# Kernel optimization log

Measured on AMD Instinct MI355X. Metric: run time of the kernel, lower is better.

Reference implementation:

```python
import jax, jax.numpy as jnp
import numpy as np
from jax import lax

NUM_CLS = 58

def _bsign(a):
    # BNN sign: +1 for a >= 0, -1 otherwise
    return jnp.where(a >= 0, 1.0, -1.0).astype(a.dtype)

def _conv(x, w, stride=1):
    return lax.conv_general_dilated(
        x, w, window_strides=(stride, stride), padding='VALID',
        dimension_numbers=('NCHW', 'OIHW', 'NCHW'))

def _binconv(x, w):
    # BinaryConv2d: binarize activations and weights via sign, then conv
    return _conv(_bsign(x), _bsign(w))

def _maxpool(x, k=2, s=2):
    return lax.reduce_window(x, -jnp.inf, lax.max,
                             (1, 1, k, k), (1, 1, s, s), 'VALID')

def setup_inputs() -> dict:
    key = jax.random.key(0)
    ks = jax.random.split(key, 7)
    B = 1024
    x = jax.random.normal(ks[0], (B, 3, 32, 32), dtype=jnp.float32)
    w0 = jax.random.normal(ks[1], (128, 3, 3, 3), dtype=jnp.float32) * 0.1   # float conv
    w1 = jax.random.normal(ks[2], (128, 128, 3, 3), dtype=jnp.float32) * 0.1 # binary conv
    w2 = jax.random.normal(ks[3], (128, 128, 3, 3), dtype=jnp.float32) * 0.1 # binary conv
    w3 = jax.random.normal(ks[4], (128, 128, 3, 3), dtype=jnp.float32) * 0.1 # binary conv
    w4 = jax.random.normal(ks[5], (128, 128, 1, 1), dtype=jnp.float32) * 0.1 # binary 1x1
    w5 = jax.random.normal(ks[6], (NUM_CLS, 128, 1, 1), dtype=jnp.float32) * 0.1  # float 1x1
    return {'x': x, 'w0': w0, 'w1': w1, 'w2': w2, 'w3': w3, 'w4': w4, 'w5': w5}

def reference(x, w0, w1, w2, w3, w4, w5):
    # features
    h = _conv(x, w0)            # [B,128,30,30]
    h = _maxpool(h, 2, 2)       # [B,128,15,15]
    h = _binconv(h, w1)         # [B,128,13,13]
    h = _maxpool(h, 2, 2)       # [B,128,6,6]
    h = _binconv(h, w2)         # [B,128,4,4]
    h = _maxpool(h, 2, 1)       # [B,128,3,3]
    # classifier
    h = _binconv(h, w3)         # [B,128,1,1]
    h = _binconv(h, w4)         # [B,128,1,1]
    h = jax.nn.relu(h)
    h = _conv(h, w5)            # [B,58,1,1]
    return jax.nn.softmax(h, axis=1)
```

## Files before the change

kernel.cpp:

```cpp
#include <hip/hip_runtime.h>
#include <cmath>

#define NUM_CLS 58

typedef _Float16 v8h __attribute__((ext_vector_type(8)));
typedef float v4f __attribute__((ext_vector_type(4)));
typedef int v4i __attribute__((ext_vector_type(4)));
union HU { v8h h; uint4 u; };

__global__ __launch_bounds__(256) void prep_all(
    const float* __restrict__ w0, const float* __restrict__ w1,
    const float* __restrict__ w2, const float* __restrict__ w3,
    const float* __restrict__ w4,
    unsigned long long* __restrict__ wb3, unsigned long long* __restrict__ wb4,
    _Float16* __restrict__ bsig, _Float16* __restrict__ babs,
    uint4* __restrict__ bw1f, uint4* __restrict__ bw2f) {
    int id = blockIdx.x, tid = threadIdx.x;
    int lane = tid & 63, wv = tid >> 6;
    if (id < 128) {
        int oc = id;
        __shared__ float s[1152];
        const float* base = w3 + (size_t)oc * 1152;
        for (int i = tid; i < 1152; i += 256) s[i] = base[i];
        __syncthreads();
        for (int k = wv; k < 9; k += 4) {
            unsigned long long b0 = __ballot(s[lane * 9 + k] >= 0.f);
            unsigned long long b1 = __ballot(s[(lane + 64) * 9 + k] >= 0.f);
            if (lane == 0) { wb3[(oc * 9 + k) * 2] = b0; wb3[(oc * 9 + k) * 2 + 1] = b1; }
        }
    } else if (id < 160) {
        int oc = (id - 128) * 4 + wv;
        unsigned long long b0 = __ballot(w4[oc * 128 + lane] >= 0.f);
        unsigned long long b1 = __ballot(w4[oc * 128 + lane + 64] >= 0.f);
        if (lane == 0) { wb4[oc * 2] = b0; wb4[oc * 2 + 1] = b1; }
    } else if (id < 162) {
        int nt = (id - 160) * 4 + wv;
        int n = nt * 16 + (lane & 15);
        int k0 = (lane >> 4) * 8;
#pragma unroll
        for (int j = 0; j < 8; j++) {
            int k = k0 + j;
            float v = (k < 27) ? w0[n * 27 + k] : 0.f;
            bsig[(nt * 64 + lane) * 8 + j] = (_Float16)v;
            babs[(nt * 64 + lane) * 8 + j] = (_Float16)fabsf(v);
        }
    } else {
        bool isw1 = id < 198;
        const float* w = isw1 ? w1 : w2;
        uint4* o = isw1 ? bw1f : bw2f;
        int fi = (isw1 ? id - 162 : id - 198) * 256 + tid;
        int tk = fi >> 9;
        int rem = fi & 511;
        int nt = rem >> 6, ln = rem & 63;
        int oc = nt * 16 + (ln & 15);
        int tap = tk >> 1, kk = tk & 1;
        int icb = kk * 64 + (ln >> 4) * 16;
        const float* wp = w + (size_t)oc * 1152 + tap;
        unsigned int dd[4];
#pragma unroll
        for (int q = 0; q < 4; ++q) {
            unsigned int v = 0;
#pragma unroll
            for (int j = 0; j < 4; ++j)
                v |= (wp[(icb + q * 4 + j) * 9] >= 0.f ? 0x01u : 0xFFu) << (8 * j);
            dd[q] = v;
        }
        uint4 d; d.x = dd[0]; d.y = dd[1]; d.z = dd[2]; d.w = dd[3];
        o[fi] = d;
    }
}

union UEXP {
    struct {
        _Float16 xh[3172];
        alignas(16) uint4 bfrag[512];
    } p0;
    unsigned char expb[225 * 128];
    struct {
        alignas(16) unsigned char expb2[36 * 128];
        unsigned short sgn2[16 * 8];
    } p2;
};
union BS {
    alignas(16) unsigned long long bits1[450];
    unsigned short sgn1[144 * 8];
};

__global__ __launch_bounds__(256, 4) void fused_net(
    const float* __restrict__ x, const float* __restrict__ w0,
    const _Float16* __restrict__ bsigG, const _Float16* __restrict__ babsG,
    const uint4* __restrict__ bw1f, const uint4* __restrict__ bw2f,
    const unsigned long long* __restrict__ wb3, const unsigned long long* __restrict__ wb4,
    const float* __restrict__ w5, float* __restrict__ out) {
    __shared__ UEXP u;
    __shared__ BS bs;
    __shared__ unsigned int lut[16];
    __shared__ unsigned long long bits3[18];
    __shared__ unsigned long long bits4[2];
    __shared__ float r_s[128];
    __shared__ float l_s[NUM_CLS];
    __shared__ float e_s[NUM_CLS];
    __shared__ unsigned int qcnt;
    __shared__ unsigned int queue[256];

    int b = blockIdx.x;
    int tid = threadIdx.x;
    int lane = tid & 63, wave = tid >> 6;
    const float* xb = x + (size_t)b * 3072;
    (void)babsG;

    if (tid < 16) {
        unsigned int v = 0;
#pragma unroll
        for (int j = 0; j < 4; ++j) v |= (((tid >> j) & 1) ? 0x01u : 0xFFu) << (8 * j);
        lut[tid] = v;
    }

    {
        for (int i = tid; i < 3072; i += 256) {
            int c = i >> 10, rem = i & 1023;
            u.p0.xh[c * 1057 + (rem >> 5) * 33 + (rem & 31)] = (_Float16)xb[i];
        }
        const uint4* bs4 = (const uint4*)bsigG;
        for (int i = tid; i < 512; i += 256) u.p0.bfrag[i] = bs4[i];
        if (tid == 0) qcnt = 0;

        int k0 = (lane >> 4) * 8;
        int offj[8];
#pragma unroll
        for (int j = 0; j < 8; j++) {
            int k = k0 + j;
            int c = k / 9, r = (k % 9) / 3, q = k % 3;
            offj[j] = c * 1057 + r * 33 + q;
        }
        unsigned short* b1u16 = (unsigned short*)bs.bits1;
        __syncthreads();

        for (int mt = wave; mt < 57; mt += 4) {
            int mg = mt * 16 + (lane & 15);
            int me = mg < 900 ? mg : 899;
            int p = me >> 2, win = me & 3;
            int py = p / 15, px = p - py * 15;
            int base = (py * 2 + (win >> 1)) * 33 + px * 2 + (win & 1);
            v8h a;
#pragma unroll
            for (int j = 0; j < 8; j++)
                a[j] = (k0 + j < 27) ? u.p0.xh[base + offj[j]] : (_Float16)0.f;
            HU ua; ua.h = a;
            ua.u.x &= 0x7FFF7FFFu; ua.u.y &= 0x7FFF7FFFu;
            ua.u.z &= 0x7FFF7FFFu; ua.u.w &= 0x7FFF7FFFu;
            int myp = mt * 4 + (lane >> 4);
#pragma unroll
            for (int nt = 0; nt < 8; nt++) {
                HU bsf; bsf.u = u.p0.bfrag[nt * 64 + lane];
                HU baf;
                baf.u.x = bsf.u.x & 0x7FFF7FFFu; baf.u.y = bsf.u.y & 0x7FFF7FFFu;
                baf.u.z = bsf.u.z & 0x7FFF7FFFu; baf.u.w = bsf.u.w & 0x7FFF7FFFu;
                v4f s  = __builtin_amdgcn_mfma_f32_16x16x32_f16(a,    bsf.h, (v4f){0.f,0.f,0.f,0.f}, 0, 0, 0);
                v4f sa = __builtin_amdgcn_mfma_f32_16x16x32_f16(ua.h, baf.h, (v4f){0.f,0.f,0.f,0.f}, 0, 0, 0);
                float bd0 = fmaf(sa[0], 1.1e-3f, 1e-5f);
                float bd1 = fmaf(sa[1], 1.1e-3f, 1e-5f);
                float bd2 = fmaf(sa[2], 1.1e-3f, 1e-5f);
                float bd3 = fmaf(sa[3], 1.1e-3f, 1e-5f);
                unsigned long long mkpos =
                    __ballot(s[0] >= bd0) | __ballot(s[1] >= bd1) |
                    __ballot(s[2] >= bd2) | __ballot(s[3] >= bd3);
                unsigned long long mkunc =
                    (__ballot(fabsf(s[0]) < bd0) | __ballot(fabsf(s[1]) < bd1) |
                     __ballot(fabsf(s[2]) < bd2) | __ballot(fabsf(s[3]) < bd3)) & ~mkpos;
                if ((lane & 15) == 0 && myp < 225)
                    b1u16[myp * 8 + nt] = (unsigned short)(mkpos >> (lane & 48));
                if (__builtin_expect(mkunc != 0ull, 0)) {
                    if (((mkunc >> lane) & 1ull) && myp < 225) {
                        unsigned int qi = atomicAdd(&qcnt, 1u);
                        if (qi < 256) queue[qi] = (unsigned)myp | ((unsigned)(nt * 16 + (lane & 15)) << 8);
                    }
                }
            }
        }
        __syncthreads();
        unsigned int nq = qcnt < 256u ? qcnt : 256u;
        for (unsigned int i = tid; i < nq; i += 256) {
            unsigned int e = queue[i];
            int p = e & 255; int oc = (e >> 8) & 255;
            int py = p / 15, px = p - py * 15;
            bool pos = false;
#pragma unroll
            for (int win = 0; win < 4; win++) {
                int base = (py * 2 + (win >> 1)) * 32 + px * 2 + (win & 1);
                double sd = 0.0;
#pragma unroll
                for (int k = 0; k < 27; k++) {
                    int c = k / 9, r = (k % 9) / 3, q = k % 3;
                    sd += (double)xb[base + c * 1024 + r * 32 + q] * (double)w0[oc * 27 + k];
                }
                pos |= (sd >= 0.0);
            }
            if (pos) atomicOr(&bs.bits1[p * 2 + (oc >> 6)], 1ull << (oc & 63));
        }
    }
    __syncthreads();

    if (tid < 225) {
        ulonglong2 bw = ((const ulonglong2*)bs.bits1)[tid];
        unsigned char* dst = u.expb + tid * 128;
        int sw = (tid & 7) << 4;
#pragma unroll
        for (int c2 = 0; c2 < 2; ++c2) {
            unsigned long long v = c2 ? bw.y : bw.x;
#pragma unroll
            for (int c = 0; c < 4; ++c) {
                uint4 d;
                d.x = lut[(v >> (c * 16 +  0)) & 15];
                d.y = lut[(v >> (c * 16 +  4)) & 15];
                d.z = lut[(v >> (c * 16 +  8)) & 15];
                d.w = lut[(v >> (c * 16 + 12)) & 15];
                *(uint4*)(dst + (((c2 * 4 + c) * 16) ^ sw)) = d;
            }
        }
    }
    __syncthreads();

    {
        int pg_[9];
#pragma unroll
        for (int mt = 0; mt < 9; ++mt) {
            int w = mt * 16 + (lane & 15);
            int wy = w / 12, wx = w - wy * 12;
            pg_[mt] = (wy * 15 + wx) * 128 + ((lane >> 4) << 4);
        }

        for (int pass = 0; pass < 2; ++pass) {
            int nt = wave * 2 + pass;
            v4i acc[9];
#pragma unroll
            for (int mt = 0; mt < 9; ++mt) acc[mt] = (v4i){0, 0, 0, 0};
#pragma unroll 2
            for (int tk = 0; tk < 18; ++tk) {
                int tap = tk >> 1, kk = tk & 1;
                int tapoff = tap + (tap / 3) * 12;
                int tks = tapoff * 128 + kk * 64;
                uint4 bfr = bw1f[(tk * 8 + nt) * 64 + lane];
                v4i bf; bf.x = (int)bfr.x; bf.y = (int)bfr.y; bf.z = (int)bfr.z; bf.w = (int)bfr.w;
#pragma unroll
                for (int mt = 0; mt < 9; ++mt) {
                    int full = pg_[mt] + tks;
                    int addr = full ^ ((full >> 3) & 0x70);
                    v4i af = *(const v4i*)(u.expb + addr);
                    acc[mt] = __builtin_amdgcn_mfma_i32_16x16x64_i8(af, bf, acc[mt], 0, 0, 0);
                }
            }
#pragma unroll
            for (int mt = 0; mt < 9; ++mt) {
#pragma unroll
                for (int r = 0; r < 4; ++r) {
                    unsigned long long mm = __ballot(acc[mt][r] >= 0);
                    if ((lane & 15) == 0)
                        bs.sgn1[(mt * 16 + (lane >> 4) * 4 + r) * 8 + nt] =
                            (unsigned short)(mm >> lane);
                }
            }
        }
    }
    __syncthreads();

    if (tid < 144) {
        int cell = tid >> 2, cg = tid & 3;
        int cy = cell / 6, cx = cell - cy * 6;
        int w0i = (2 * cy) * 12 + 2 * cx;
        int g0 = cg * 2, g1 = cg * 2 + 1;
        unsigned v0 = (unsigned)bs.sgn1[w0i * 8 + g0]        | (unsigned)bs.sgn1[(w0i + 1) * 8 + g0]
                    | (unsigned)bs.sgn1[(w0i + 12) * 8 + g0] | (unsigned)bs.sgn1[(w0i + 13) * 8 + g0];
        unsigned v1 = (unsigned)bs.sgn1[w0i * 8 + g1]        | (unsigned)bs.sgn1[(w0i + 1) * 8 + g1]
                    | (unsigned)bs.sgn1[(w0i + 12) * 8 + g1] | (unsigned)bs.sgn1[(w0i + 13) * 8 + g1];
        unsigned vv = v0 | (v1 << 16);
        int sw = (cell & 7) << 4;
        unsigned char* dst = u.p2.expb2 + cell * 128;
        uint4 d0, d1;
        d0.x = lut[vv & 15];         d0.y = lut[(vv >> 4) & 15];
        d0.z = lut[(vv >> 8) & 15];  d0.w = lut[(vv >> 12) & 15];
        d1.x = lut[(vv >> 16) & 15]; d1.y = lut[(vv >> 20) & 15];
        d1.z = lut[(vv >> 24) & 15]; d1.w = lut[(vv >> 28) & 15];
        *(uint4*)(dst + ((cg * 32) ^ sw)) = d0;
        *(uint4*)(dst + ((cg * 32 + 16) ^ sw)) = d1;
    }
    __syncthreads();

    {
        int m = lane & 15;
        int y2 = m >> 2, x2 = m & 3;
        int pg2 = (y2 * 6 + x2) * 128 + ((lane >> 4) << 4);
        int ntA = wave * 2, ntB = wave * 2 + 1;
        v4i acc0 = (v4i){0, 0, 0, 0}, acc1 = (v4i){0, 0, 0, 0};
#pragma unroll 2
        for (int tk = 0; tk < 18; ++tk) {
            int tap = tk >> 1, kk = tk & 1;
            int tapoff2 = (tap / 3) * 6 + (tap % 3);
            int tks = tapoff2 * 128 + kk * 64;
            uint4 br0 = bw2f[(tk * 8 + ntA) * 64 + lane];
            uint4 br1 = bw2f[(tk * 8 + ntB) * 64 + lane];
            v4i b0; b0.x = (int)br0.x; b0.y = (int)br0.y; b0.z = (int)br0.z; b0.w = (int)br0.w;
            v4i b1; b1.x = (int)br1.x; b1.y = (int)br1.y; b1.z = (int)br1.z; b1.w = (int)br1.w;
            int full = pg2 + tks;
            int addr = full ^ ((full >> 3) & 0x70);
            v4i af = *(const v4i*)(u.p2.expb2 + addr);
            acc0 = __builtin_amdgcn_mfma_i32_16x16x64_i8(af, b0, acc0, 0, 0, 0);
            acc1 = __builtin_amdgcn_mfma_i32_16x16x64_i8(af, b1, acc1, 0, 0, 0);
        }
#pragma unroll
        for (int r = 0; r < 4; ++r) {
            unsigned long long m0 = __ballot(acc0[r] >= 0);
            unsigned long long m1 = __ballot(acc1[r] >= 0);
            if ((lane & 15) == 0) {
                u.p2.sgn2[(((lane >> 4) * 4 + r)) * 8 + ntA] = (unsigned short)(m0 >> lane);
                u.p2.sgn2[(((lane >> 4) * 4 + r)) * 8 + ntB] = (unsigned short)(m1 >> lane);
            }
        }
    }
    __syncthreads();

    if (tid < 128) {
        int idx = tid >> 4, sh = tid & 15;
        int half = tid >> 6;
        for (int p = 0; p < 9; ++p) {
            int py = p / 3, px = p - py * 3;
            int m00 = py * 4 + px;
            unsigned v = (unsigned)u.p2.sgn2[m00 * 8 + idx]       | (unsigned)u.p2.sgn2[(m00 + 1) * 8 + idx]
                       | (unsigned)u.p2.sgn2[(m00 + 4) * 8 + idx] | (unsigned)u.p2.sgn2[(m00 + 5) * 8 + idx];
            unsigned long long mm = __ballot(((v >> sh) & 1u) != 0u);
            if ((tid & 63) == 0) bits3[p * 2 + half] = mm;
        }
    }
    __syncthreads();

    if (tid < 128) {
        int P = 0;
#pragma unroll
        for (int k = 0; k < 9; k++) {
            P += __popcll(bits3[k * 2] ^ wb3[tid * 18 + k * 2]);
            P += __popcll(bits3[k * 2 + 1] ^ wb3[tid * 18 + k * 2 + 1]);
        }
        unsigned long long m = __ballot(P <= 576);
        if ((tid & 63) == 0) bits4[tid >> 6] = m;
    }
    __syncthreads();
    if (tid < 128) {
        unsigned long long i0 = bits4[0], i1 = bits4[1];
        int v = 128 - 2 * (int)(__popcll(i0 ^ wb4[tid * 2]) + __popcll(i1 ^ wb4[tid * 2 + 1]));
        r_s[tid] = v > 0 ? (float)v : 0.f;
    }
    __syncthreads();
    if (tid < NUM_CLS) {
        float l = 0.f;
#pragma unroll 8
        for (int k = 0; k < 128; k++) l = fmaf(w5[tid * 128 + k], r_s[k], l);
        l_s[tid] = l;
    }
    __syncthreads();
    if (tid < NUM_CLS) {
        float mx = -1e30f;
        for (int k = 0; k < NUM_CLS; k++) mx = fmaxf(mx, l_s[k]);
        e_s[tid] = expf(l_s[tid] - mx);
    }
    __syncthreads();
    if (tid < NUM_CLS) {
        float sum = 0.f;
        for (int k = 0; k < NUM_CLS; k++) sum += e_s[k];
        out[(size_t)b * NUM_CLS + tid] = e_s[tid] / sum;
    }
}

extern "C" void kernel_launch(void* const* d_in, const int* in_sizes, int n_in,
                              void* d_out, int out_size, void* d_ws, size_t ws_size,
                              hipStream_t stream) {
    const float* x  = (const float*)d_in[0];
    const float* w0 = (const float*)d_in[1];
    const float* w1 = (const float*)d_in[2];
    const float* w2 = (const float*)d_in[3];
    const float* w3 = (const float*)d_in[4];
    const float* w4 = (const float*)d_in[5];
    const float* w5 = (const float*)d_in[6];
    float* out = (float*)d_out;

    int B = in_sizes[0] / 3072;

    size_t off = 0;
    auto carve = [&](size_t bytes) {
        void* p = (char*)d_ws + off;
        off += (bytes + 255) & ~(size_t)255;
        return p;
    };
    unsigned long long* wb3 = (unsigned long long*)carve(1152 * 2 * 8);
    unsigned long long* wb4 = (unsigned long long*)carve(128 * 2 * 8);
    _Float16* bsig = (_Float16*)carve(8 * 64 * 8 * 2);
    _Float16* babs = (_Float16*)carve(8 * 64 * 8 * 2);
    uint4* bw1f = (uint4*)carve(18 * 8 * 64 * 16);
    uint4* bw2f = (uint4*)carve(18 * 8 * 64 * 16);
    (void)ws_size; (void)n_in; (void)out_size;

    prep_all<<<234, 256, 0, stream>>>(w0, w1, w2, w3, w4, wb3, wb4, bsig, babs, bw1f, bw2f);
    fused_net<<<B, 256, 0, stream>>>(x, w0, bsig, babs, bw1f, bw2f, wb3, wb4, w5, out);
}
```

Before: 132.6 us.

## Restructure conv1 MFMA loop to share A fragments across two N tiles

The binary conv1 MFMA loop used to run two passes over the N tiles, each reloading all 9 M-tile A fragments from LDS. It now processes both N tiles together in three groups of three M tiles, so each A fragment load feeds two MFMAs. The aim is to halve LDS reads of the activation fragments and give the scheduler more independent MFMAs. The cost is three extra loads of the small B fragment stream, and register pressure stays about the same (6 accumulators instead of 9).

Result: no change. 133.4 us (+0.6%).

```diff
diff --git a/kernel.cpp b/kernel.cpp
--- a/kernel.cpp
+++ b/kernel.cpp
@@ -7,6 +7,7 @@
 typedef float v4f __attribute__((ext_vector_type(4)));
 typedef int v4i __attribute__((ext_vector_type(4)));
 union HU { v8h h; uint4 u; };
+template<int N> struct IC { static constexpr int value = N; };
 
 __global__ __launch_bounds__(256) void prep_all(
     const float* __restrict__ w0, const float* __restrict__ w1,
@@ -222,45 +223,54 @@
     __syncthreads();
 
     {
-        int pg_[9];
-#pragma unroll
-        for (int mt = 0; mt < 9; ++mt) {
-            int w = mt * 16 + (lane & 15);
-            int wy = w / 12, wx = w - wy * 12;
-            pg_[mt] = (wy * 15 + wx) * 128 + ((lane >> 4) << 4);
-        }
-
-        for (int pass = 0; pass < 2; ++pass) {
-            int nt = wave * 2 + pass;
-            v4i acc[9];
-#pragma unroll
-            for (int mt = 0; mt < 9; ++mt) acc[mt] = (v4i){0, 0, 0, 0};
+        int ntA = wave * 2, ntB = wave * 2 + 1;
+        auto run3 = [&](auto G_C) {
+            constexpr int G = G_C.value;
+            v4i acc0[3], acc1[3];
+            int pg[3];
+#pragma unroll
+            for (int m = 0; m < 3; ++m) {
+                acc0[m] = (v4i){0, 0, 0, 0};
+                acc1[m] = (v4i){0, 0, 0, 0};
+                int w = (G * 3 + m) * 16 + (lane & 15);
+                int wy = w / 12, wx = w - wy * 12;
+                pg[m] = (wy * 15 + wx) * 128 + ((lane >> 4) << 4);
+            }
 #pragma unroll 2
             for (int tk = 0; tk < 18; ++tk) {
                 int tap = tk >> 1, kk = tk & 1;
                 int tapoff = tap + (tap / 3) * 12;
                 int tks = tapoff * 128 + kk * 64;
-                uint4 bfr = bw1f[(tk * 8 + nt) * 64 + lane];
-                v4i bf; bf.x = (int)bfr.x; bf.y = (int)bfr.y; bf.z = (int)bfr.z; bf.w = (int)bfr.w;
-#pragma unroll
-                for (int mt = 0; mt < 9; ++mt) {
-                    int full = pg_[mt] + tks;
+                uint4 br0 = bw1f[(tk * 8 + ntA) * 64 + lane];
+                uint4 br1 = bw1f[(tk * 8 + ntB) * 64 + lane];
+                v4i b0; b0.x = (int)br0.x; b0.y = (int)br0.y; b0.z = (int)br0.z; b0.w = (int)br0.w;
+                v4i b1; b1.x = (int)br1.x; b1.y = (int)br1.y; b1.z = (int)br1.z; b1.w = (int)br1.w;
+#pragma unroll
+                for (int m = 0; m < 3; ++m) {
+                    int full = pg[m] + tks;
                     int addr = full ^ ((full >> 3) & 0x70);
                     v4i af = *(const v4i*)(u.expb + addr);
-                    acc[mt] = __builtin_amdgcn_mfma_i32_16x16x64_i8(af, bf, acc[mt], 0, 0, 0);
+                    acc0[m] = __builtin_amdgcn_mfma_i32_16x16x64_i8(af, b0, acc0[m], 0, 0, 0);
+                    acc1[m] = __builtin_amdgcn_mfma_i32_16x16x64_i8(af, b1, acc1[m], 0, 0, 0);
                 }
             }
 #pragma unroll
-            for (int mt = 0; mt < 9; ++mt) {
+            for (int m = 0; m < 3; ++m) {
+                int mt = G * 3 + m;
 #pragma unroll
                 for (int r = 0; r < 4; ++r) {
-                    unsigned long long mm = __ballot(acc[mt][r] >= 0);
-                    if ((lane & 15) == 0)
-                        bs.sgn1[(mt * 16 + (lane >> 4) * 4 + r) * 8 + nt] =
-                            (unsigned short)(mm >> lane);
+                    unsigned long long m0 = __ballot(acc0[m][r] >= 0);
+                    unsigned long long m1 = __ballot(acc1[m][r] >= 0);
+                    if ((lane & 15) == 0) {
+                        bs.sgn1[(mt * 16 + (lane >> 4) * 4 + r) * 8 + ntA] = (unsigned short)(m0 >> lane);
+                        bs.sgn1[(mt * 16 + (lane >> 4) * 4 + r) * 8 + ntB] = (unsigned short)(m1 >> lane);
+                    }
                 }
             }
-        }
+        };
+        run3(IC<0>{});
+        run3(IC<1>{});
+        run3(IC<2>{});
     }
     __syncthreads();
 
```
